# Optimization experiments

Measured on AMD Instinct MI355X. Metric: run time of the kernel, lower is better.

Reference implementation:

```python
import jax, jax.numpy as jnp
import numpy as np

TEMPERATURE = 10000.0
LN_EPS = 1e-5

def build_freqs(H, W, head_dim):
    # (H*W, head_dim) rotary angles: [theta_h, theta_h, theta_w, theta_w]
    gh, gw = jnp.meshgrid(jnp.arange(H, dtype=jnp.float32), jnp.arange(W, dtype=jnp.float32), indexing='ij')
    dq = head_dim // 4
    freq = 1.0 / (TEMPERATURE ** (jnp.arange(dq, dtype=jnp.float32) / dq))
    th = gh.reshape(-1, 1) * freq[None, :]
    tw = gw.reshape(-1, 1) * freq[None, :]
    return jnp.concatenate([th, th, tw, tw], axis=-1)

def apply_rope(x, freqs):
    # x: (B, nh, N, hd), freqs: (N, hd)
    cos = jnp.cos(freqs)[None, None]
    sin = jnp.sin(freqs)[None, None]
    hd = x.shape[-1]
    x1, x2 = x[..., :hd // 2], x[..., hd // 2:]
    x_rot = jnp.concatenate([-x2, x1], axis=-1)
    return x * cos + x_rot * sin

def setup_inputs() -> dict:
    key = jax.random.key(0)
    ks = jax.random.split(key, 8)
    dim, hidden, B, H, W = 192, 384, 4, 128, 128
    N = H * W
    s = 0.02
    return {
        'x': jax.random.normal(ks[0], (B, N, dim), jnp.float32),
        'in_w': jax.random.normal(ks[1], (hidden, dim), jnp.float32) * s,
        'in_b': jnp.zeros((hidden,), jnp.float32),
        'qkv_w': jax.random.normal(ks[2], (3 * hidden, hidden), jnp.float32) * s,
        'qkv_b': jnp.zeros((3 * hidden,), jnp.float32),
        'lepe_w': jax.random.normal(ks[3], (hidden, 1, 3, 3), jnp.float32) * s,
        'lepe_b': jnp.zeros((hidden,), jnp.float32),
        'ln_g': jnp.ones((hidden,), jnp.float32),
        'ln_b': jnp.zeros((hidden,), jnp.float32),
        'out_w': jax.random.normal(ks[4], (dim, hidden), jnp.float32) * s,
        'out_b': jnp.zeros((dim,), jnp.float32),
        'H': H,
        'W': W,
    }

def reference(x, in_w, in_b, qkv_w, qkv_b, lepe_w, lepe_b, ln_g, ln_b, out_w, out_b, H, W):
    B, N, C = x.shape
    hidden = in_w.shape[0]
    nh = 8
    hd = hidden // nh
    # in_proj: 1x1 conv == per-token linear
    x_seq = jnp.einsum('bnc,hc->bnh', x, in_w) + in_b
    # fused qkv
    qkv = jnp.einsum('bnh,oh->bno', x_seq, qkv_w) + qkv_b
    q, k, v = jnp.split(qkv, 3, axis=-1)
    # LEPE: 3x3 depthwise conv on V in NCHW layout
    v2d = v.transpose(0, 2, 1).reshape(B, hidden, H, W)
    lepe = jax.lax.conv_general_dilated(
        v2d, lepe_w, window_strides=(1, 1), padding=((1, 1), (1, 1)),
        feature_group_count=hidden, dimension_numbers=('NCHW', 'OIHW', 'NCHW'))
    lepe = lepe + lepe_b[None, :, None, None]
    v = v + lepe.reshape(B, hidden, N).transpose(0, 2, 1)
    # split heads -> (B, nh, N, hd)
    q = q.reshape(B, N, nh, hd).transpose(0, 2, 1, 3)
    k = k.reshape(B, N, nh, hd).transpose(0, 2, 1, 3)
    v = v.reshape(B, N, nh, hd).transpose(0, 2, 1, 3)
    freqs = build_freqs(H, W, hd)
    q = apply_rope(q, freqs)
    k = apply_rope(k, freqs)
    # phi = ELU + 1 feature map
    q = jax.nn.elu(q) + 1.0
    k = jax.nn.elu(k) + 1.0
    # linear attention associativity trick
    kv = jnp.einsum('bhnd,bhne->bhde', k, v)
    out = jnp.einsum('bhnd,bhde->bhne', q, kv)
    k_sum = k.sum(axis=2)  # (B, nh, hd)
    denom = jnp.maximum(jnp.einsum('bhnd,bhd->bhn', q, k_sum)[..., None], 1e-6)
    out = out / denom
    out = out.transpose(0, 2, 1, 3).reshape(B, N, hidden)
    # LayerNorm + out_proj
    mu = out.mean(axis=-1, keepdims=True)
    var = out.var(axis=-1, keepdims=True)
    out = (out - mu) * jax.lax.rsqrt(var + LN_EPS) * ln_g + ln_b
    return jnp.einsum('bnh,ch->bnc', out, out_w) + out_b
```

## Files before the change

kernel.cpp:

```cpp
#include <hip/hip_runtime.h>
#include <cstdint>
#include <cstddef>

#define NN_TOK 16384
#define ROWS   65536
#define CDIM   192
#define HID    384
#define NHEAD  8
#define HD     48
#define QKVO   1152

typedef unsigned short ushort_t;
typedef __bf16 bf16x8 __attribute__((ext_vector_type(8)));
typedef float  f32x4  __attribute__((ext_vector_type(4)));

__device__ __forceinline__ ushort_t f2bf(float f) {
  unsigned int u = __float_as_uint(f);
  u += 0x7fffu + ((u >> 16) & 1u);
  return (ushort_t)(u >> 16);
}
__device__ __forceinline__ float bf2f(ushort_t u) {
  return __uint_as_float(((unsigned int)u) << 16);
}

__global__ void cast_x(const float* __restrict__ x, ushort_t* __restrict__ xb, int n8) {
  int i = blockIdx.x * blockDim.x + threadIdx.x;
  if (i >= n8) return;
  const float4* src = (const float4*)(x + (size_t)i * 8);
  float4 f0 = src[0], f1 = src[1];
  uint4 pk;
  pk.x = (unsigned)f2bf(f0.x) | ((unsigned)f2bf(f0.y) << 16);
  pk.y = (unsigned)f2bf(f0.z) | ((unsigned)f2bf(f0.w) << 16);
  pk.z = (unsigned)f2bf(f1.x) | ((unsigned)f2bf(f1.y) << 16);
  pk.w = (unsigned)f2bf(f1.z) | ((unsigned)f2bf(f1.w) << 16);
  *(uint4*)(xb + (size_t)i * 8) = pk;
}

__global__ void combine_w(const float* __restrict__ in_w, const float* __restrict__ in_b,
                          const float* __restrict__ qkv_w, const float* __restrict__ qkv_b,
                          ushort_t* __restrict__ Wcb, float* __restrict__ bc) {
  int o = blockIdx.x;
  int c = threadIdx.x;
  const float* qw = qkv_w + o * HID;
  float s = 0.f;
  for (int m = 0; m < HID; ++m) s += qw[m] * in_w[m * CDIM + c];
  Wcb[o * CDIM + c] = f2bf(s);
  if (c == 0) {
    float sb = qkv_b[o];
    for (int m = 0; m < HID; ++m) sb += qw[m] * in_b[m];
    bc[o] = sb;
  }
}

__global__ void cast_ow(const float* __restrict__ w, ushort_t* __restrict__ wb, int n) {
  int i = blockIdx.x * blockDim.x + threadIdx.x;
  if (i < n) wb[i] = f2bf(w[i]);
}

__global__ void build_tab(float4* __restrict__ tab4) {
  int i = blockIdx.x * blockDim.x + threadIdx.x;
  if (i >= NN_TOK * 24) return;
  int n = i / 24, dp = i - n * 24;
  int j = dp % 12;
  const float c0 = 1.1073093649624542f;
  float freq = exp2f(-(float)j * c0);
  float fy = (float)(n >> 7), fx = (float)(n & 127);
  float s1, c1, s2, c2;
  sincosf(fy * freq, &s1, &c1);
  sincosf(fx * freq, &s2, &c2);
  tab4[i] = make_float4(c1, s1, c2, s2);
}

template<int BM, int BN, int WM, int WN, bool OUTBF16>
__global__ __launch_bounds__(256) void gemm_mfma(const ushort_t* __restrict__ A, int lda,
                                                 const ushort_t* __restrict__ Wb,
                                                 const float* __restrict__ bias,
                                                 void* __restrict__ Cptr,
                                                 int K, int O, int nbx) {
  constexpr int TM = BM / WM / 16;
  constexpr int TN = BN / WN / 16;
  __shared__ __align__(16) ushort_t As[BM][40];
  __shared__ __align__(16) ushort_t Bs[BN][40];
  const int t    = threadIdx.x;
  const int lane = t & 63;
  const int wave = t >> 6;
  const int quad = lane >> 4;
  const int l15  = lane & 15;
  const int wm   = wave / WN, wn = wave % WN;
  const int m_base = wm * (BM / WM);
  const int n_base = wn * (BN / WN);
  const int cpx = gridDim.x >> 3;
  const int id  = blockIdx.x;
  const int swz = (id & 7) * cpx + (id >> 3);
  const int o0  = (swz % nbx) * BN;
  const int n0  = (swz / nbx) * BM;
  f32x4 acc[TM][TN] = {};

  for (int kt = 0; kt < K; kt += 32) {
    for (int c = t; c < BM * 4; c += 256) {
      int row = c >> 2, col8 = (c & 3) * 8;
      *(uint4*)&As[row][col8] = *(const uint4*)(A + (size_t)(n0 + row) * lda + kt + col8);
    }
    for (int c = t; c < BN * 4; c += 256) {
      int row = c >> 2, col8 = (c & 3) * 8;
      *(uint4*)&Bs[row][col8] = *(const uint4*)(Wb + (size_t)(o0 + row) * K + kt + col8);
    }
    __syncthreads();
    bf16x8 af[TM], bfr[TN];
#pragma unroll
    for (int mi = 0; mi < TM; ++mi)
      af[mi] = *(const bf16x8*)&As[m_base + mi * 16 + l15][quad * 8];
#pragma unroll
    for (int ni = 0; ni < TN; ++ni)
      bfr[ni] = *(const bf16x8*)&Bs[n_base + ni * 16 + l15][quad * 8];
#pragma unroll
    for (int mi = 0; mi < TM; ++mi)
#pragma unroll
      for (int ni = 0; ni < TN; ++ni)
        acc[mi][ni] = __builtin_amdgcn_mfma_f32_16x16x32_bf16(af[mi], bfr[ni], acc[mi][ni], 0, 0, 0);
    __syncthreads();
  }
#pragma unroll
  for (int mi = 0; mi < TM; ++mi) {
#pragma unroll
    for (int ni = 0; ni < TN; ++ni) {
      int col = o0 + n_base + ni * 16 + l15;
      float bv = bias[col];
      int rbase = n0 + m_base + mi * 16 + quad * 4;
#pragma unroll
      for (int r = 0; r < 4; ++r) {
        float val = acc[mi][ni][r] + bv;
        if (OUTBF16) ((ushort_t*)Cptr)[(size_t)(rbase + r) * O + col] = f2bf(val);
        else         ((float*)Cptr)[(size_t)(rbase + r) * O + col] = val;
      }
    }
  }
}

__device__ __forceinline__ int fragEl(int pg, int nb, int dd, int nm) {
  return pg * 2200 + nb * 136 + dd * 8 + nm;
}

__global__ __launch_bounds__(256) void kv_partial_k(const ushort_t* __restrict__ kq,
                                                    const ushort_t* __restrict__ vq,
                                                    const float4* __restrict__ tab4,
                                                    const float* __restrict__ lw,
                                                    const float* __restrict__ lb,
                                                    float* __restrict__ part) {
  const int bid   = blockIdx.x;
  const int chunk = bid & 63;
  const int bh    = bid >> 6;
  const int b     = bh >> 3;
  const int h     = bh & 7;
  const int t     = threadIdx.x;
  const int lane  = t & 63;
  const int wave  = t >> 6;
  __shared__ __align__(16) ushort_t ksR[3 * 2200];
  __shared__ __align__(16) ushort_t vsR[4 * 2200];
  __shared__ __align__(16) float wlds[9][48];
  __shared__ __align__(16) float blds[48];
  float* red = (float*)&ksR[0];
  for (int c = t; c < 432; c += 256) {
    int ch = c / 9, tap = c - ch * 9;
    wlds[tap][ch] = lw[(h * HD + ch) * 9 + tap];
  }
  if (t < 48) blds[t] = lb[h * HD + t];
  for (int c = t; c < 2048; c += 256) {
    int nb = c >> 7, dd = (c >> 3) & 15, nm = c & 7;
    vsR[fragEl(3, nb, dd, nm)] = (dd == 0) ? (ushort_t)0x3F80 : (ushort_t)0;
  }
  __syncthreads();

  const int g  = lane >> 4;
  const int d0 = lane & 15;
  f32x4 acc[3][4] = {};
  const int n0 = b * NN_TOK + chunk * 256;

  for (int it = 0; it < 2; ++it) {
    const int nbase = it * 128;
    for (int c = t; c < 384; c += 256) {
      int rr = c / 3, s8 = (c - (c / 3) * 3) * 8;
      int n  = n0 + nbase + rr;
      int nn = n & (NN_TOK - 1);
      const ushort_t* kr = kq + (size_t)n * QKVO + h * HD;
      uint4 ka = *(const uint4*)(kr + s8);
      uint4 kb = *(const uint4*)(kr + s8 + 24);
      ushort_t ua[8], ub[8];
      *(uint4*)ua = ka; *(uint4*)ub = kb;
      const float4* t4 = tab4 + nn * 24 + s8;
      const int nb = rr >> 3, nm = rr & 7;
#pragma unroll
      for (int jj = 0; jj < 8; ++jj) {
        float4 cs = t4[jj];
        float in1 = bf2f(ua[jj]), in2 = bf2f(ub[jj]);
        float o1 = in1 * cs.x - in2 * cs.y;
        float o2 = in2 * cs.z + in1 * cs.w;
        o1 = (o1 > 0.f) ? o1 + 1.f : expf(o1);
        o2 = (o2 > 0.f) ? o2 + 1.f : expf(o2);
        const int d1 = s8 + jj, d2 = s8 + 24 + jj;
        ksR[fragEl(d1 >> 4, nb, d1 & 15, nm)] = f2bf(o1);
        ksR[fragEl(d2 >> 4, nb, d2 & 15, nm)] = f2bf(o2);
      }
    }
    {
      const int nst = chunk * 256 + nbase;
      const int y   = nst >> 7;
      for (int c = t; c < 768; c += 256) {
        int rr = c / 6, gg = c - (c / 6) * 6;
        int x = rr;
        float a8[8], ctr[8];
        *(float4*)&a8[0] = *(const float4*)&blds[gg * 8];
        *(float4*)&a8[4] = *(const float4*)&blds[gg * 8 + 4];
#pragma unroll
        for (int dy = -1; dy <= 1; ++dy) {
#pragma unroll
          for (int dx = -1; dx <= 1; ++dx) {
            int yy = y + dy, xx = x + dx;
            bool inb = ((unsigned)yy < 128u) && ((unsigned)xx < 128u);
            int yc = min(max(yy, 0), 127), xc = min(max(xx, 0), 127);
            const ushort_t* src = vq + ((size_t)(b * NN_TOK + (yc << 7) + xc)) * QKVO + h * HD + gg * 8;
            uint4 pk = *(const uint4*)src;
            if (!inb) pk = make_uint4(0u, 0u, 0u, 0u);
            const int tap = (dy + 1) * 3 + (dx + 1);
            float wt[8];
            *(float4*)&wt[0] = *(const float4*)&wlds[tap][gg * 8];
            *(float4*)&wt[4] = *(const float4*)&wlds[tap][gg * 8 + 4];
            ushort_t uu[8];
            *(uint4*)uu = pk;
#pragma unroll
            for (int ci = 0; ci < 8; ++ci) {
              float val = bf2f(uu[ci]);
              if (dy == 0 && dx == 0) ctr[ci] = val;
              a8[ci] += wt[ci] * val;
            }
          }
        }
        const int nb = rr >> 3, nm = rr & 7;
#pragma unroll
        for (int ci = 0; ci < 8; ++ci) {
          const int e = gg * 8 + ci;
          vsR[fragEl(e >> 4, nb, e & 15, nm)] = f2bf(ctr[ci] + a8[ci]);
        }
      }
    }
    __syncthreads();
    {
      const int w4 = wave * 4 + g;
      bf16x8 af[3], bfr[4];
#pragma unroll
      for (int dg = 0; dg < 3; ++dg) af[dg]  = *(const bf16x8*)&ksR[fragEl(dg, w4, d0, 0)];
#pragma unroll
      for (int eg = 0; eg < 4; ++eg) bfr[eg] = *(const bf16x8*)&vsR[fragEl(eg, w4, d0, 0)];
#pragma unroll
      for (int dg = 0; dg < 3; ++dg)
#pragma unroll
        for (int eg = 0; eg < 4; ++eg)
          acc[dg][eg] = __builtin_amdgcn_mfma_f32_16x16x32_bf16(af[dg], bfr[eg], acc[dg][eg], 0, 0, 0);
    }
    __syncthreads();
  }
  if (wave == 0) {
#pragma unroll
    for (int dg = 0; dg < 3; ++dg)
#pragma unroll
      for (int eg = 0; eg < 4; ++eg)
#pragma unroll
        for (int r = 0; r < 4; ++r)
          red[(dg * 16 + g * 4 + r) * 64 + eg * 16 + d0] = acc[dg][eg][r];
  }
  __syncthreads();
  for (int w = 1; w < 4; ++w) {
    if (wave == w) {
#pragma unroll
      for (int dg = 0; dg < 3; ++dg)
#pragma unroll
        for (int eg = 0; eg < 4; ++eg)
#pragma unroll
          for (int r = 0; r < 4; ++r)
            red[(dg * 16 + g * 4 + r) * 64 + eg * 16 + d0] += acc[dg][eg][r];
    }
    __syncthreads();
  }
  float* p = part + (size_t)bid * 2352;
  for (int c = t; c < 2352; c += 256) {
    int d = c / 49, e = c - d * 49;
    p[c] = red[d * 64 + e];
  }
}

__global__ void kv_phase2(const float* __restrict__ part, ushort_t* __restrict__ kvT) {
  int bh  = blockIdx.x >> 3;
  int seg = blockIdx.x & 7;
  int t   = threadIdx.x;
  ushort_t* dst = kvT + (size_t)bh * 8192;
  for (int i = seg * 1024 + t; i < (seg + 1) * 1024; i += 256) {
    int rem = i & 4095, e = rem >> 6, d = rem & 63;
    if (d >= 48 || e >= 49) dst[i] = 0;
  }
  int cend = (seg + 1) * 294;
  for (int c = seg * 294 + t; c < cend; c += 256) {
    const float* p = part + (size_t)(bh * 64) * 2352 + c;
    float s = 0.f;
    for (int ch = 0; ch < 64; ++ch) s += p[(size_t)ch * 2352];
    int d = c / 49, e = c - d * 49;
    ushort_t hi = f2bf(s);
    float lo = s - bf2f(hi);
    dst[(size_t)e * 64 + d]        = hi;
    dst[4096 + (size_t)e * 64 + d] = f2bf(lo);
  }
}

__global__ __launch_bounds__(256) void attn_ln_fused(const ushort_t* __restrict__ q,
                                                     const float4* __restrict__ tab4,
                                                     const ushort_t* __restrict__ kvT,
                                                     const float* __restrict__ ln_g,
                                                     const float* __restrict__ ln_b,
                                                     ushort_t* __restrict__ oln) {
  __shared__ __align__(16) ushort_t qsL[32][392];
  __shared__ float lnp[4][32][2];
  const int t    = threadIdx.x;
  const int lane = t & 63;
  const int wave = t >> 6;
  const int quad = lane >> 4;
  const int l15  = lane & 15;
  const int row0 = blockIdx.x * 32;
  const int b    = row0 >> 14;
  const int h0   = wave * 2;
  const float2* tab2 = (const float2*)tab4;

  for (int c = t; c < 1536; c += 256) {
    int r = c / 48, seg = c - (c / 48) * 48;
    *(uint4*)&qsL[r][seg * 8] = *(const uint4*)(q + (size_t)(row0 + r) * QKVO + seg * 8);
  }
  __syncthreads();

  f32x4 acc[2][2][4] = {};

  float gg[2][3], bb[2][3];
#pragma unroll
  for (int hi = 0; hi < 2; ++hi)
#pragma unroll
    for (int nt = 0; nt < 3; ++nt) {
      int col = (h0 + hi) * 48 + nt * 16 + l15;
      gg[hi][nt] = ln_g[col];
      bb[hi][nt] = ln_b[col];
    }

#pragma unroll
  for (int s = 0; s < 2; ++s) {
    const int d0 = s * 32 + quad * 8;
    const bool valid = d0 < 48;
    const bool caseA = d0 < 24;
    const int dp0 = caseA ? d0 : d0 - 24;
    bf16x8 af[2][2] = {};
    if (valid) {
      const int dpart = caseA ? d0 + 24 : d0 - 24;
      const int csel  = caseA ? 0 : 1;
      const float sgn = caseA ? -1.f : 1.f;
#pragma unroll
      for (int m = 0; m < 2; ++m) {
        const int r  = row0 + m * 16 + l15;
        const int nn = r & (NN_TOK - 1);
        float2 cs[8];
#pragma unroll
        for (int j = 0; j < 8; ++j) cs[j] = tab2[(size_t)(nn * 24 + dp0 + j) * 2 + csel];
#pragma unroll
        for (int hi = 0; hi < 2; ++hi) {
          const ushort_t* qr = &qsL[m * 16 + l15][(h0 + hi) * 48];
          uint4 pr = *(const uint4*)(qr + d0);
          uint4 pa = *(const uint4*)(qr + dpart);
          ushort_t up[8], ua[8];
          *(uint4*)up = pr; *(uint4*)ua = pa;
          unsigned w[4];
#pragma unroll
          for (int j2 = 0; j2 < 4; ++j2) {
            float o2[2];
#pragma unroll
            for (int k = 0; k < 2; ++k) {
              int j = j2 * 2 + k;
              float vp = bf2f(up[j]), va = bf2f(ua[j]);
              float o = vp * cs[j].x + va * (sgn * cs[j].y);
              o2[k] = (o > 0.f) ? o + 1.f : expf(o);
            }
            w[j2] = (unsigned)f2bf(o2[0]) | ((unsigned)f2bf(o2[1]) << 16);
          }
          uint4 pk = make_uint4(w[0], w[1], w[2], w[3]);
          af[hi][m] = *(bf16x8*)&pk;
        }
      }
    }
#pragma unroll
    for (int hi = 0; hi < 2; ++hi) {
      const ushort_t* kb = kvT + (size_t)(b * 8 + h0 + hi) * 8192;
#pragma unroll
      for (int nt = 0; nt < 4; ++nt) {
        bf16x8 bH = *(const bf16x8*)(kb + (nt * 16 + l15) * 64 + d0);
        bf16x8 bL = *(const bf16x8*)(kb + 4096 + (nt * 16 + l15) * 64 + d0);
#pragma unroll
        for (int m = 0; m < 2; ++m) {
          acc[hi][m][nt] = __builtin_amdgcn_mfma_f32_16x16x32_bf16(af[hi][m], bH, acc[hi][m][nt], 0, 0, 0);
          acc[hi][m][nt] = __builtin_amdgcn_mfma_f32_16x16x32_bf16(af[hi][m], bL, acc[hi][m][nt], 0, 0, 0);
        }
      }
    }
  }

  float rdn[2][2][4];
#pragma unroll
  for (int hi = 0; hi < 2; ++hi)
#pragma unroll
    for (int m = 0; m < 2; ++m)
#pragma unroll
      for (int r = 0; r < 4; ++r) {
        float dn = __shfl(acc[hi][m][3][r], lane & 48);
        rdn[hi][m][r] = 1.f / fmaxf(dn, 1e-6f);
      }
  float s1[2][4] = {}, s2[2][4] = {};
#pragma unroll
  for (int hi = 0; hi < 2; ++hi)
#pragma unroll
    for (int m = 0; m < 2; ++m)
#pragma unroll
      for (int nt = 0; nt < 3; ++nt)
#pragma unroll
        for (int r = 0; r < 4; ++r) {
          float o = acc[hi][m][nt][r] * rdn[hi][m][r];
          acc[hi][m][nt][r] = o;
          s1[m][r] += o;
          s2[m][r] += o * o;
        }
#pragma unroll
  for (int m = 0; m < 2; ++m)
#pragma unroll
    for (int r = 0; r < 4; ++r) {
#pragma unroll
      for (int msk = 1; msk < 16; msk <<= 1) {
        s1[m][r] += __shfl_xor(s1[m][r], msk, 64);
        s2[m][r] += __shfl_xor(s2[m][r], msk, 64);
      }
    }
  if (l15 == 0) {
#pragma unroll
    for (int m = 0; m < 2; ++m)
#pragma unroll
      for (int r = 0; r < 4; ++r) {
        int rr = m * 16 + quad * 4 + r;
        lnp[wave][rr][0] = s1[m][r];
        lnp[wave][rr][1] = s2[m][r];
      }
  }
  __syncthreads();
  float muv[2][4], rsv[2][4];
#pragma unroll
  for (int m = 0; m < 2; ++m)
#pragma unroll
    for (int r = 0; r < 4; ++r) {
      int rr = m * 16 + quad * 4 + r;
      float a  = lnp[0][rr][0] + lnp[1][rr][0] + lnp[2][rr][0] + lnp[3][rr][0];
      float bq = lnp[0][rr][1] + lnp[1][rr][1] + lnp[2][rr][1] + lnp[3][rr][1];
      float mu  = a * (1.f / 384.f);
      float var = bq * (1.f / 384.f) - mu * mu;
      muv[m][r] = mu;
      rsv[m][r] = rsqrtf(var + 1e-5f);
    }
#pragma unroll
  for (int hi = 0; hi < 2; ++hi)
#pragma unroll
    for (int m = 0; m < 2; ++m)
#pragma unroll
      for (int nt = 0; nt < 3; ++nt) {
        int col = (h0 + hi) * 48 + nt * 16 + l15;
#pragma unroll
        for (int r = 0; r < 4; ++r) {
          int rr = m * 16 + quad * 4 + r;
          float v = (acc[hi][m][nt][r] - muv[m][r]) * rsv[m][r] * gg[hi][nt] + bb[hi][nt];
          qsL[rr][col] = f2bf(v);
        }
      }
  __syncthreads();
  for (int c = t; c < 1536; c += 256) {
    int r = c / 48, seg = c - (c / 48) * 48;
    *(uint4*)(oln + (size_t)(row0 + r) * QKVO + seg * 8) = *(const uint4*)&qsL[r][seg * 8];
  }
}

extern "C" void kernel_launch(void* const* d_in, const int* in_sizes, int n_in,
                              void* d_out, int out_size, void* d_ws, size_t ws_size,
                              hipStream_t stream) {
  const float* x      = (const float*)d_in[0];
  const float* in_w   = (const float*)d_in[1];
  const float* in_b   = (const float*)d_in[2];
  const float* qkv_w  = (const float*)d_in[3];
  const float* qkv_b  = (const float*)d_in[4];
  const float* lepe_w = (const float*)d_in[5];
  const float* lepe_b = (const float*)d_in[6];
  const float* ln_g   = (const float*)d_in[7];
  const float* ln_b   = (const float*)d_in[8];
  const float* out_w  = (const float*)d_in[9];
  const float* out_b  = (const float*)d_in[10];
  float* out = (float*)d_out;

  float*    ws     = (float*)d_ws;
  float*    qkvbF  = ws;
  float*    xbF    = qkvbF + (size_t)ROWS * QKVO / 2;
  float*    WcbF   = xbF   + (size_t)ROWS * CDIM / 2;
  float*    bc     = WcbF  + (size_t)QKVO * CDIM / 2;
  float*    owbF   = bc    + QKVO;
  float*    tab4F  = owbF  + (size_t)CDIM * HID / 2;
  ushort_t* qkvb   = (ushort_t*)qkvbF;
  ushort_t* xb     = (ushort_t*)xbF;
  float*    part   = xbF;
  ushort_t* kvT    = (ushort_t*)(xbF + (size_t)2048 * 2352);
  ushort_t* Wcb    = (ushort_t*)WcbF;
  ushort_t* owb    = (ushort_t*)owbF;
  float4*   tab4   = (float4*)tab4F;

  cast_x<<<(ROWS * CDIM / 8 + 255) / 256, 256, 0, stream>>>(x, xb, ROWS * CDIM / 8);
  combine_w<<<QKVO, CDIM, 0, stream>>>(in_w, in_b, qkv_w, qkv_b, Wcb, bc);
  cast_ow<<<(CDIM * HID + 255) / 256, 256, 0, stream>>>(out_w, owb, CDIM * HID);
  build_tab<<<(NN_TOK * 24 + 255) / 256, 256, 0, stream>>>(tab4);

  gemm_mfma<128, 128, 2, 2, true><<<4608, 256, 0, stream>>>(
      xb, CDIM, Wcb, bc, qkvb, CDIM, QKVO, 9);

  kv_partial_k<<<2048, 256, 0, stream>>>(qkvb + HID, qkvb + 2 * HID, tab4, lepe_w, lepe_b, part);
  kv_phase2<<<256, 256, 0, stream>>>(part, kvT);

  attn_ln_fused<<<ROWS / 32, 256, 0, stream>>>(qkvb, tab4, kvT, ln_g, ln_b, qkvb + HID);

  gemm_mfma<128, 64, 4, 1, false><<<1536, 256, 0, stream>>>(
      qkvb + HID, QKVO, owb, out_b, out, HID, CDIM, 3);
}
```

Measured before the change: 416.0 us.

## Fuse out_proj GEMM into attention+LayerNorm kernel epilogue

The output projection is now computed inside attn_ln_fused using MFMA on the LayerNorm result held in LDS, and fp32 output is written directly. This removes the separate out_proj GEMM launch and the bf16 round trip of the normalized activations through global memory. The out_w weights are pre-permuted into the MFMA fragment layout so each lane can load its B fragments with one vector load. In exchange, each block rereads the full 192x384 weight from global/L2 and does more work per block, which may raise register pressure.

```diff
diff --git a/kernel.cpp b/kernel.cpp
--- a/kernel.cpp
+++ b/kernel.cpp
@@ -52,9 +52,15 @@
   }
 }
 
-__global__ void cast_ow(const float* __restrict__ w, ushort_t* __restrict__ wb, int n) {
+__global__ void cast_owT(const float* __restrict__ w, ushort_t* __restrict__ wt, int n) {
   int i = blockIdx.x * blockDim.x + threadIdx.x;
-  if (i < n) wb[i] = f2bf(w[i]);
+  if (i >= n) return;
+  int j = i & 7, rest = i >> 3;
+  int l15 = rest & 15; rest >>= 4;
+  int quad = rest & 3; rest >>= 2;
+  int kt = rest % 12, ct = rest / 12;
+  int col = ct * 16 + l15, k = kt * 32 + quad * 8 + j;
+  wt[i] = f2bf(w[col * HID + k]);
 }
 
 __global__ void build_tab(float4* __restrict__ tab4) {
@@ -315,7 +321,9 @@
                                                      const ushort_t* __restrict__ kvT,
                                                      const float* __restrict__ ln_g,
                                                      const float* __restrict__ ln_b,
-                                                     ushort_t* __restrict__ oln) {
+                                                     const ushort_t* __restrict__ owbT,
+                                                     const float* __restrict__ out_b,
+                                                     float* __restrict__ outp) {
   __shared__ __align__(16) ushort_t qsL[32][392];
   __shared__ float lnp[4][32][2];
   const int t    = threadIdx.x;
@@ -478,9 +486,41 @@
         }
       }
   __syncthreads();
+
+  f32x4 oac[2][3] = {};
+  const int ct0 = wave * 3;
+  for (int kt = 0; kt < 12; ++kt) {
+    bf16x8 af2[2];
+    af2[0] = *(const bf16x8*)&qsL[l15][kt * 32 + quad * 8];
+    af2[1] = *(const bf16x8*)&qsL[16 + l15][kt * 32 + quad * 8];
+    bf16x8 bfr2[3];
+#pragma unroll
+    for (int nt = 0; nt < 3; ++nt)
+      bfr2[nt] = *(const bf16x8*)&owbT[(size_t)((((ct0 + nt) * 12 + kt) * 4 + quad) * 16 + l15) * 8];
+#pragma unroll
+    for (int m2 = 0; m2 < 2; ++m2)
+#pragma unroll
+      for (int nt = 0; nt < 3; ++nt)
+        oac[m2][nt] = __builtin_amdgcn_mfma_f32_16x16x32_bf16(af2[m2], bfr2[nt], oac[m2][nt], 0, 0, 0);
+  }
+  float obv[3];
+#pragma unroll
+  for (int nt = 0; nt < 3; ++nt) obv[nt] = out_b[ct0 * 16 + nt * 16 + l15];
+  __syncthreads();
+  float* coL = (float*)&qsL[0][0];
+#pragma unroll
+  for (int m2 = 0; m2 < 2; ++m2)
+#pragma unroll
+    for (int nt = 0; nt < 3; ++nt) {
+      int col = ct0 * 16 + nt * 16 + l15;
+#pragma unroll
+      for (int r = 0; r < 4; ++r)
+        coL[(m2 * 16 + quad * 4 + r) * 196 + col] = oac[m2][nt][r] + obv[nt];
+    }
+  __syncthreads();
   for (int c = t; c < 1536; c += 256) {
     int r = c / 48, seg = c - (c / 48) * 48;
-    *(uint4*)(oln + (size_t)(row0 + r) * QKVO + seg * 8) = *(const uint4*)&qsL[r][seg * 8];
+    *(float4*)(outp + (size_t)(row0 + r) * CDIM + seg * 4) = *(const float4*)&coL[r * 196 + seg * 4];
   }
 }
 
@@ -512,12 +552,12 @@
   float*    part   = xbF;
   ushort_t* kvT    = (ushort_t*)(xbF + (size_t)2048 * 2352);
   ushort_t* Wcb    = (ushort_t*)WcbF;
-  ushort_t* owb    = (ushort_t*)owbF;
+  ushort_t* owbT   = (ushort_t*)owbF;
   float4*   tab4   = (float4*)tab4F;
 
   cast_x<<<(ROWS * CDIM / 8 + 255) / 256, 256, 0, stream>>>(x, xb, ROWS * CDIM / 8);
   combine_w<<<QKVO, CDIM, 0, stream>>>(in_w, in_b, qkv_w, qkv_b, Wcb, bc);
-  cast_ow<<<(CDIM * HID + 255) / 256, 256, 0, stream>>>(out_w, owb, CDIM * HID);
+  cast_owT<<<(CDIM * HID + 255) / 256, 256, 0, stream>>>(out_w, owbT, CDIM * HID);
   build_tab<<<(NN_TOK * 24 + 255) / 256, 256, 0, stream>>>(tab4);
 
   gemm_mfma<128, 128, 2, 2, true><<<4608, 256, 0, stream>>>(
@@ -526,8 +566,5 @@
   kv_partial_k<<<2048, 256, 0, stream>>>(qkvb + HID, qkvb + 2 * HID, tab4, lepe_w, lepe_b, part);
   kv_phase2<<<256, 256, 0, stream>>>(part, kvT);
 
-  attn_ln_fused<<<ROWS / 32, 256, 0, stream>>>(qkvb, tab4, kvT, ln_g, ln_b, qkvb + HID);
-
-  gemm_mfma<128, 64, 4, 1, false><<<1536, 256, 0, stream>>>(
-      qkvb + HID, QKVO, owb, out_b, out, HID, CDIM, 3);
-}
+  attn_ln_fused<<<ROWS / 32, 256, 0, stream>>>(qkvb, tab4, kvT, ln_g, ln_b, owbT, out_b, out);
+}
```

Result: faster. 398.8 us (-4.2%).
